# Kernel tuning notes

Hardware: AMD Instinct MI355X
Metric: run time of the kernel (lower is better)

The kernel has to match this reference:

```python
import jax, jax.numpy as jnp
import numpy as np


def lstm_step(x_t, h, c, Wih, Whh, bih, bhh):
    # PyTorch LSTM gate order: i, f, g, o
    gates = x_t @ Wih.T + h @ Whh.T + bih + bhh
    i, f, g, o = jnp.split(gates, 4, axis=-1)
    i = jax.nn.sigmoid(i)
    f = jax.nn.sigmoid(f)
    g = jnp.tanh(g)
    o = jax.nn.sigmoid(o)
    c_new = f * c + i * g
    h_new = o * jnp.tanh(c_new)
    return h_new, c_new


def setup_inputs() -> dict:
    key = jax.random.key(0)
    N, C, T, V, M = 512, 3, 300, 25, 2
    F = C * V * M  # 150
    H = 100
    ks = jax.random.split(key, 12)
    s = 1.0 / np.sqrt(H)  # PyTorch LSTM/Linear init scale
    u = lambda k, shape: jax.random.uniform(k, shape, jnp.float32, -s, s)
    return {
        "x": jax.random.normal(ks[0], (N, C, T, V, M), jnp.float32),
        "enc_Wih": u(ks[1], (4 * H, F)),
        "enc_Whh": u(ks[2], (4 * H, H)),
        "enc_bih": u(ks[3], (4 * H,)),
        "enc_bhh": u(ks[4], (4 * H,)),
        "dec_Wih": u(ks[5], (4 * H, F)),
        "dec_Whh": u(ks[6], (4 * H, H)),
        "dec_bih": u(ks[7], (4 * H,)),
        "dec_bhh": u(ks[8], (4 * H,)),
        "fc_W": u(ks[9], (F, H)),
        "fc_b": u(ks[10], (F,)),
    }


def reference(x, enc_Wih, enc_Whh, enc_bih, enc_bhh,
              dec_Wih, dec_Whh, dec_bih, dec_bhh, fc_W, fc_b):
    N, C, T, V, M = x.shape
    F = C * V * M
    H = enc_Whh.shape[1]
    # (N,C,T,V,M) -> (N,T,C*V*M)
    xs = jnp.transpose(x, (0, 2, 1, 3, 4)).reshape(N, T, F)

    # Encoder LSTM: only need final (h, c)
    h0 = jnp.zeros((N, H), x.dtype)
    c0 = jnp.zeros((N, H), x.dtype)

    def enc_step(carry, xt):
        h, c = carry
        h, c = lstm_step(xt, h, c, enc_Wih, enc_Whh, enc_bih, enc_bhh)
        return (h, c), None

    (h, c), _ = jax.lax.scan(enc_step, (h0, c0), jnp.swapaxes(xs, 0, 1))

    inp0 = jnp.zeros((N, F), x.dtype)

    def dec_step(carry, _):
        inp, h, c = carry
        h, c = lstm_step(inp, h, c, dec_Wih, dec_Whh, dec_bih, dec_bhh)
        out = h @ fc_W.T + fc_b
        return (out, h, c), out

    _, outs = jax.lax.scan(dec_step, (inp0, h, c), None, length=T - 1)  # [T-1,N,F]

    # outputs[:,0,:] stays zero, like the torch.zeros buffer
    outputs = jnp.concatenate([jnp.zeros((1, N, F), x.dtype), outs], axis=0)  # [T,N,F]
    outputs = jnp.swapaxes(outputs, 0, 1).reshape(N, T, C, V, M)
    return jnp.transpose(outputs, (0, 2, 1, 3, 4))  # (N,C,T,V,M)
```

## Files before the change

kernel.cpp:

```cpp
#include <hip/hip_runtime.h>
#include <hip/hip_fp16.h>


#define OFF_W2T   0
#define OFF_WDT   51200
#define OFF_WET   102400
#define OFF_PIH   153600
#define OFF_BENC  192000
#define OFF_B1    192512
#define OFF_BEFF  193024
#define OFF_HIST  193536
#define HIST_STRIDE 29952
#define OFF_XG    7861248

typedef _Float16 h2_t __attribute__((ext_vector_type(2)));

#if defined(__has_builtin)
#if __has_builtin(__builtin_amdgcn_fdot2)
#define HAS_FDOT2 1
#endif
#endif

__device__ __forceinline__ float fdot2u(unsigned a, unsigned b, float c) {
#ifdef HAS_FDOT2
  return __builtin_amdgcn_fdot2(__builtin_bit_cast(h2_t, a), __builtin_bit_cast(h2_t, b), c, false);
#else
  float al = __half2float(__ushort_as_half((unsigned short)(a & 0xffffu)));
  float ah = __half2float(__ushort_as_half((unsigned short)(a >> 16)));
  float bl = __half2float(__ushort_as_half((unsigned short)(b & 0xffffu)));
  float bh = __half2float(__ushort_as_half((unsigned short)(b >> 16)));
  return fmaf(ah, bh, fmaf(al, bl, c));
#endif
}

__device__ __forceinline__ float fast_sig(float x) {
  float e = __builtin_amdgcn_exp2f(x * -1.442695040888963f);
  return __builtin_amdgcn_rcpf(1.f + e);
}
__device__ __forceinline__ float fast_tanh(float x) {
  float e = __builtin_amdgcn_exp2f(x * -2.885390081777926f);
  return fmaf(2.f, __builtin_amdgcn_rcpf(1.f + e), -1.f);
}

__device__ __forceinline__ float lstm_tail(float acc, int ty, float& c) {
  float v1 = __shfl_xor(acc, 1);
  float v2 = __shfl_xor(acc, 2);
  float v3 = __shfl_xor(v1, 2);
  float d0 = acc;
  float iv = (ty==0)?d0:(ty==1)?v1:(ty==2)?v2:v3;
  float fv = (ty==1)?d0:(ty==0)?v1:(ty==3)?v2:v3;
  float gv = (ty==2)?d0:(ty==3)?v1:(ty==0)?v2:v3;
  float ov = (ty==3)?d0:(ty==2)?v1:(ty==1)?v2:v3;
  float fi = fast_sig(iv), ff = fast_sig(fv), fo = fast_sig(ov);
  float fg = fast_tanh(gv);
  c = fmaf(ff, c, fi * fg);
  return fo * fast_tanh(c);
}

__global__ void prep(const float* __restrict__ dWih, const float* __restrict__ dWhh,
                     const float* __restrict__ dbih, const float* __restrict__ dbhh,
                     const float* __restrict__ eWih, const float* __restrict__ eWhh,
                     const float* __restrict__ ebih, const float* __restrict__ ebhh,
                     const float* __restrict__ fcW,  const float* __restrict__ fcb,
                     float* __restrict__ ws)
{
  int idx = blockIdx.x * 256 + threadIdx.x;
  if (idx < 51200) {
    int j = idx >> 9, t = idx & 511;
    float w2 = 0.f, wd = 0.f, we = 0.f;
    if (t < 400) {
      int r = (t & 3) * 100 + (t >> 2);
      float s = dWhh[r * 100 + j];
      float acc = 0.f;
      for (int f = 0; f < 150; ++f) acc = fmaf(dWih[r * 150 + f], fcW[f * 100 + j], acc);
      w2 = s + acc; wd = s; we = eWhh[r * 100 + j];
    }
    ws[OFF_W2T + idx] = w2; ws[OFF_WDT + idx] = wd; ws[OFF_WET + idx] = we;
  } else if (idx < 51200 + 38400) {
    int k = idx - 51200; int d = k >> 9, t = k & 511;
    unsigned pk = 0;
    if (t < 400) {
      int r = (t & 3) * 100 + (t >> 2);
      unsigned lo = __half_as_ushort(__float2half(eWih[r * 150 + 2 * d]));
      unsigned hi = __half_as_ushort(__float2half(eWih[r * 150 + 2 * d + 1]));
      pk = lo | (hi << 16);
    }
    ((unsigned*)ws)[OFF_PIH + k] = pk;
  } else if (idx < 51200 + 38400 + 512) {
    int t = idx - (51200 + 38400);
    float be = 0.f, b1 = 0.f, bf = 0.f;
    if (t < 400) {
      int r = (t & 3) * 100 + (t >> 2);
      be = ebih[r] + ebhh[r];
      b1 = dbih[r] + dbhh[r];
      float acc = 0.f;
      for (int f = 0; f < 150; ++f) acc = fmaf(dWih[r * 150 + f], fcb[f], acc);
      bf = b1 + acc;
    }
    ws[OFF_BENC + t] = be; ws[OFF_B1 + t] = b1; ws[OFF_BEFF + t] = bf;
  }
}

__global__ __launch_bounds__(512, 4)
void pre(const float* __restrict__ x, const float* __restrict__ ws,
         unsigned short* __restrict__ xg, int n0)
{
  const int tid = threadIdx.x;
  const int n = n0 + blockIdx.x;
  __shared__ unsigned short xls[150 * 160];

  unsigned wih[75];
  const unsigned* pih = ((const unsigned*)ws) + OFF_PIH;
#pragma unroll
  for (int d = 0; d < 75; ++d) wih[d] = pih[(d << 9) + tid];

  const float* xb = x + (size_t)n * 45000;
  unsigned short* xgr = xg + (size_t)blockIdx.x * 120000 + ((tid < 400) ? tid : 0);
  const bool on = tid < 400;

  for (int phase = 0; phase < 2; ++phase) {
    const int tbase = phase * 150;
    if (phase) __syncthreads();
    for (int d = tid; d < 150 * 160; d += 512) {
      int tl = d / 160, f = d - tl * 160;
      float v = 0.f;
      if (f < 150) {
        int c = f / 50, q = f - c * 50;
        v = xb[c * 15000 + (tbase + tl) * 50 + q];
      }
      xls[tl * 160 + f] = __half_as_ushort(__float2half(v));
    }
    __syncthreads();
    if (on) {
      for (int tl = 0; tl < 150; ++tl) {
        const uint4* row = (const uint4*)(xls + tl * 160);
        float a = 0.f;
#pragma unroll
        for (int ch = 0; ch < 18; ++ch) {
          uint4 v = row[ch];
          a = fdot2u(wih[4 * ch + 0], v.x, a);
          a = fdot2u(wih[4 * ch + 1], v.y, a);
          a = fdot2u(wih[4 * ch + 2], v.z, a);
          a = fdot2u(wih[4 * ch + 3], v.w, a);
        }
        uint4 v = row[18];
        a = fdot2u(wih[72], v.x, a);
        a = fdot2u(wih[73], v.y, a);
        a = fdot2u(wih[74], v.z, a);
        xgr[(size_t)(tbase + tl) * 400] = __half_as_ushort(__float2half(a));
      }
    }
  }
}

__global__ __launch_bounds__(512, 4)
void recurrent(const unsigned short* __restrict__ xg, float* __restrict__ ws, int n0)
{
  const int t  = threadIdx.x;
  const int n  = n0 + blockIdx.x;
  const int j  = t >> 2, ty = t & 3;
  const bool leader = (t < 400) && (ty == 0);
  __shared__ float hbuf[2][112];

  float whh[100];
#pragma unroll
  for (int k = 0; k < 100; ++k) whh[k] = ws[OFF_WET + (k << 9) + t];

  const float benc  = ws[OFF_BENC + t];
  const float b1g   = ws[OFF_B1   + t];
  const float beffg = ws[OFF_BEFF + t];
  unsigned short* histn = ((unsigned short*)(ws + OFF_HIST)) + (size_t)n * HIST_STRIDE;
  const unsigned short* xgr = xg + (size_t)blockIdx.x * 120000 + ((t < 400) ? t : 0);
  float c = 0.f;

  unsigned short p0 = xgr[0], p1 = xgr[400];
  for (int ts = 0; ts < 300; ++ts) {
    const int rd = ts & 1, wr = rd ^ 1;
    const int pi = (ts + 2 < 300) ? (ts + 2) : 299;
    unsigned short nx = xgr[(size_t)pi * 400];
    float acc = benc + __half2float(__ushort_as_half(p0));
    if (ts > 0) {
#pragma unroll
      for (int k = 0; k < 100; k += 4) {
        float4 h4 = *(const float4*)&hbuf[rd][k];
        acc = fmaf(whh[k+0], h4.x, acc);
        acc = fmaf(whh[k+1], h4.y, acc);
        acc = fmaf(whh[k+2], h4.z, acc);
        acc = fmaf(whh[k+3], h4.w, acc);
      }
    }
    float hn = lstm_tail(acc, ty, c);
    if (leader) hbuf[wr][j] = hn;
    __syncthreads();
    p0 = p1; p1 = nx;
  }

#pragma unroll
  for (int k = 0; k < 100; ++k) whh[k] = ws[OFF_WDT + (k << 9) + t];
  for (int s = 1; s <= 299; ++s) {
    const int rd = (299 + s) & 1, wr = rd ^ 1;
    float acc = (s == 1) ? b1g : beffg;
#pragma unroll
    for (int k = 0; k < 100; k += 4) {
      float4 h4 = *(const float4*)&hbuf[rd][k];
      acc = fmaf(whh[k+0], h4.x, acc);
      acc = fmaf(whh[k+1], h4.y, acc);
      acc = fmaf(whh[k+2], h4.z, acc);
      acc = fmaf(whh[k+3], h4.w, acc);
    }
    float hn = lstm_tail(acc, ty, c);
    if (leader) {
      hbuf[wr][j] = hn;
      histn[(s - 1) * 100 + j] = __half_as_ushort(__float2half(hn));
    }
    __syncthreads();
    if (s == 1) {
#pragma unroll
      for (int k = 0; k < 100; ++k) whh[k] = ws[OFF_W2T + (k << 9) + t];
    }
  }
}

__global__ __launch_bounds__(192, 4)
void emit(const float* __restrict__ ws, const float* __restrict__ fcW,
          const float* __restrict__ fcb, float* __restrict__ out)
{
  const int f = threadIdx.x;
  const int n = blockIdx.x;
  const int z = blockIdx.y;
  __shared__ unsigned short hl[15008];

  const uint4* src = (const uint4*)(((const unsigned short*)(ws + OFF_HIST)) +
                                    (size_t)n * HIST_STRIDE + z * 15000);
  for (int k = f; k < 1875; k += 192) ((uint4*)hl)[k] = src[k];

  const bool on = f < 150;
  unsigned fw[50];
  float bias = 0.f;
  if (on) {
    const float* fp = fcW + f * 100;
#pragma unroll
    for (int q = 0; q < 50; ++q) {
      unsigned lo = __half_as_ushort(__float2half(fp[2*q]));
      unsigned hi = __half_as_ushort(__float2half(fp[2*q+1]));
      fw[q] = lo | (hi << 16);
    }
    bias = fcb[f];
  }
  __syncthreads();

  if (!on) return;
  const int cc = f / 50, r = f - cc * 50;
  float* ob = out + (size_t)n * 45000 + cc * 15000 + r;
  if (z == 0) ob[0] = 0.f;
  const int rows = z ? 149 : 150;
  for (int tl = 0; tl < rows; ++tl) {
    const uint4* row = (const uint4*)(hl + tl * 100);
    float acc = bias;
#pragma unroll
    for (int ch = 0; ch < 12; ++ch) {
      uint4 v = row[ch];
      acc = fdot2u(fw[4*ch+0], v.x, acc);
      acc = fdot2u(fw[4*ch+1], v.y, acc);
      acc = fdot2u(fw[4*ch+2], v.z, acc);
      acc = fdot2u(fw[4*ch+3], v.w, acc);
    }
    uint2 v2 = *(const uint2*)(hl + tl * 100 + 96);
    acc = fdot2u(fw[48], v2.x, acc);
    acc = fdot2u(fw[49], v2.y, acc);
    const int tt = z * 150 + tl + 1;
    ob[tt * 50] = acc;
  }
}

extern "C" void kernel_launch(void* const* d_in, const int* in_sizes, int n_in,
                              void* d_out, int out_size, void* d_ws, size_t ws_size,
                              hipStream_t stream) {
  const float* x    = (const float*)d_in[0];
  const float* eWih = (const float*)d_in[1];
  const float* eWhh = (const float*)d_in[2];
  const float* ebih = (const float*)d_in[3];
  const float* ebhh = (const float*)d_in[4];
  const float* dWih = (const float*)d_in[5];
  const float* dWhh = (const float*)d_in[6];
  const float* dbih = (const float*)d_in[7];
  const float* dbhh = (const float*)d_in[8];
  const float* fcW  = (const float*)d_in[9];
  const float* fcb  = (const float*)d_in[10];
  float* out = (float*)d_out;
  float* ws  = (float*)d_ws;

  const size_t fixed_bytes = (size_t)OFF_XG * 4;
  int npass = 1;
  while (npass < 8) {
    size_t need = fixed_bytes + (size_t)(512 / npass) * 300 * 400 * 2;
    if (need <= ws_size) break;
    npass *= 2;
  }
  const int chunk = 512 / npass;
  unsigned short* xg = (unsigned short*)((char*)d_ws + fixed_bytes);

  prep<<<352, 256, 0, stream>>>(dWih, dWhh, dbih, dbhh, eWih, eWhh, ebih, ebhh, fcW, fcb, ws);
  for (int p = 0; p < npass; ++p) {
    pre<<<chunk, 512, 0, stream>>>(x, ws, xg, p * chunk);
    recurrent<<<chunk, 512, 0, stream>>>(xg, ws, p * chunk);
  }
  emit<<<dim3(512, 2), 192, 0, stream>>>(ws, fcW, fcb, out);
}
```

Baseline: 1.325 ms.

## Use packed fp16 dot2 for recurrent matvec and split accumulators

Recurrent weights are stored as packed fp16 pairs and the hidden state is kept in fp16 shared memory, so each step's 100-wide matvec uses fdot2 with four independent accumulators instead of 100 serial fp32 FMAs. The LSTM tail now applies the gate nonlinearity once per lane before shuffling, instead of every lane computing all four. The first encoder step and first decoder step are peeled out of their loops, and the pre and emit dot products also get split accumulators. This halves weight register use and shortens the serial dependency chain on the per-step critical path. The cost is fp16 rounding of the hidden state and weights across 600 recurrent steps, which can build up error.

```diff
diff --git a/kernel.cpp b/kernel.cpp
--- a/kernel.cpp
+++ b/kernel.cpp
@@ -2,16 +2,16 @@
 #include <hip/hip_fp16.h>
 
 
-#define OFF_W2T   0
-#define OFF_WDT   51200
-#define OFF_WET   102400
-#define OFF_PIH   153600
-#define OFF_BENC  192000
-#define OFF_B1    192512
-#define OFF_BEFF  193024
-#define OFF_HIST  193536
+#define B_W2P   0u
+#define B_WDP   102400u
+#define B_WEP   204800u
+#define B_PIH   307200u
+#define B_BENC  460800u
+#define B_B1    462848u
+#define B_BEFF  464896u
+#define B_HIST  466944u
 #define HIST_STRIDE 29952
-#define OFF_XG    7861248
+#define B_XG    31137792u
 
 typedef _Float16 h2_t __attribute__((ext_vector_type(2)));
 
@@ -33,6 +33,11 @@
 #endif
 }
 
+__device__ __forceinline__ unsigned pack2f(float a, float b) {
+  return (unsigned)__half_as_ushort(__float2half(a)) |
+         ((unsigned)__half_as_ushort(__float2half(b)) << 16);
+}
+
 __device__ __forceinline__ float fast_sig(float x) {
   float e = __builtin_amdgcn_exp2f(x * -1.442695040888963f);
   return __builtin_amdgcn_rcpf(1.f + e);
@@ -43,18 +48,31 @@
 }
 
 __device__ __forceinline__ float lstm_tail(float acc, int ty, float& c) {
-  float v1 = __shfl_xor(acc, 1);
-  float v2 = __shfl_xor(acc, 2);
+  float sg = fast_sig(acc);
+  float th = fast_tanh(acc);
+  float act = (ty == 2) ? th : sg;
+  float v1 = __shfl_xor(act, 1);
+  float v2 = __shfl_xor(act, 2);
   float v3 = __shfl_xor(v1, 2);
-  float d0 = acc;
-  float iv = (ty==0)?d0:(ty==1)?v1:(ty==2)?v2:v3;
-  float fv = (ty==1)?d0:(ty==0)?v1:(ty==3)?v2:v3;
-  float gv = (ty==2)?d0:(ty==3)?v1:(ty==0)?v2:v3;
-  float ov = (ty==3)?d0:(ty==2)?v1:(ty==1)?v2:v3;
-  float fi = fast_sig(iv), ff = fast_sig(fv), fo = fast_sig(ov);
-  float fg = fast_tanh(gv);
-  c = fmaf(ff, c, fi * fg);
-  return fo * fast_tanh(c);
+  c = fmaf(v1, c, act * v2);
+  return v3 * fast_tanh(c);
+}
+
+__device__ __forceinline__ float dot100(const unsigned short* hb, const unsigned* wp) {
+  const uint4* h4 = (const uint4*)hb;
+  float a0 = 0.f, a1 = 0.f, a2 = 0.f, a3 = 0.f;
+#pragma unroll
+  for (int ch = 0; ch < 12; ++ch) {
+    uint4 v = h4[ch];
+    a0 = fdot2u(wp[4 * ch + 0], v.x, a0);
+    a1 = fdot2u(wp[4 * ch + 1], v.y, a1);
+    a2 = fdot2u(wp[4 * ch + 2], v.z, a2);
+    a3 = fdot2u(wp[4 * ch + 3], v.w, a3);
+  }
+  uint2 v2 = *(const uint2*)(hb + 96);
+  a0 = fdot2u(wp[48], v2.x, a0);
+  a1 = fdot2u(wp[49], v2.y, a1);
+  return (a0 + a1) + (a2 + a3);
 }
 
 __global__ void prep(const float* __restrict__ dWih, const float* __restrict__ dWhh,
@@ -62,32 +80,40 @@
                      const float* __restrict__ eWih, const float* __restrict__ eWhh,
                      const float* __restrict__ ebih, const float* __restrict__ ebhh,
                      const float* __restrict__ fcW,  const float* __restrict__ fcb,
-                     float* __restrict__ ws)
+                     char* __restrict__ wsb)
 {
   int idx = blockIdx.x * 256 + threadIdx.x;
-  if (idx < 51200) {
-    int j = idx >> 9, t = idx & 511;
-    float w2 = 0.f, wd = 0.f, we = 0.f;
+  if (idx < 25600) {
+    int q = idx >> 9, t = idx & 511;
+    unsigned w2p = 0, wdp = 0, wep = 0;
     if (t < 400) {
       int r = (t & 3) * 100 + (t >> 2);
-      float s = dWhh[r * 100 + j];
-      float acc = 0.f;
-      for (int f = 0; f < 150; ++f) acc = fmaf(dWih[r * 150 + f], fcW[f * 100 + j], acc);
-      w2 = s + acc; wd = s; we = eWhh[r * 100 + j];
-    }
-    ws[OFF_W2T + idx] = w2; ws[OFF_WDT + idx] = wd; ws[OFF_WET + idx] = we;
-  } else if (idx < 51200 + 38400) {
-    int k = idx - 51200; int d = k >> 9, t = k & 511;
+      int j0 = 2 * q, j1 = 2 * q + 1;
+      float wd0 = dWhh[r * 100 + j0], wd1 = dWhh[r * 100 + j1];
+      float we0 = eWhh[r * 100 + j0], we1 = eWhh[r * 100 + j1];
+      float s0 = 0.f, s1 = 0.f;
+      for (int f = 0; f < 150; ++f) {
+        float a = dWih[r * 150 + f];
+        s0 = fmaf(a, fcW[f * 100 + j0], s0);
+        s1 = fmaf(a, fcW[f * 100 + j1], s1);
+      }
+      w2p = pack2f(wd0 + s0, wd1 + s1);
+      wdp = pack2f(wd0, wd1);
+      wep = pack2f(we0, we1);
+    }
+    ((unsigned*)(wsb + B_W2P))[idx] = w2p;
+    ((unsigned*)(wsb + B_WDP))[idx] = wdp;
+    ((unsigned*)(wsb + B_WEP))[idx] = wep;
+  } else if (idx < 25600 + 38400) {
+    int k = idx - 25600; int d = k >> 9, t = k & 511;
     unsigned pk = 0;
     if (t < 400) {
       int r = (t & 3) * 100 + (t >> 2);
-      unsigned lo = __half_as_ushort(__float2half(eWih[r * 150 + 2 * d]));
-      unsigned hi = __half_as_ushort(__float2half(eWih[r * 150 + 2 * d + 1]));
-      pk = lo | (hi << 16);
-    }
-    ((unsigned*)ws)[OFF_PIH + k] = pk;
-  } else if (idx < 51200 + 38400 + 512) {
-    int t = idx - (51200 + 38400);
+      pk = pack2f(eWih[r * 150 + 2 * d], eWih[r * 150 + 2 * d + 1]);
+    }
+    ((unsigned*)(wsb + B_PIH))[k] = pk;
+  } else if (idx < 25600 + 38400 + 512) {
+    int t = idx - (25600 + 38400);
     float be = 0.f, b1 = 0.f, bf = 0.f;
     if (t < 400) {
       int r = (t & 3) * 100 + (t >> 2);
@@ -97,12 +123,14 @@
       for (int f = 0; f < 150; ++f) acc = fmaf(dWih[r * 150 + f], fcb[f], acc);
       bf = b1 + acc;
     }
-    ws[OFF_BENC + t] = be; ws[OFF_B1 + t] = b1; ws[OFF_BEFF + t] = bf;
+    ((float*)(wsb + B_BENC))[t] = be;
+    ((float*)(wsb + B_B1))[t]   = b1;
+    ((float*)(wsb + B_BEFF))[t] = bf;
   }
 }
 
 __global__ __launch_bounds__(512, 4)
-void pre(const float* __restrict__ x, const float* __restrict__ ws,
+void pre(const float* __restrict__ x, const char* __restrict__ wsb,
          unsigned short* __restrict__ xg, int n0)
 {
   const int tid = threadIdx.x;
@@ -110,7 +138,7 @@
   __shared__ unsigned short xls[150 * 160];
 
   unsigned wih[75];
-  const unsigned* pih = ((const unsigned*)ws) + OFF_PIH;
+  const unsigned* pih = (const unsigned*)(wsb + B_PIH);
 #pragma unroll
   for (int d = 0; d < 75; ++d) wih[d] = pih[(d << 9) + tid];
 
@@ -134,19 +162,20 @@
     if (on) {
       for (int tl = 0; tl < 150; ++tl) {
         const uint4* row = (const uint4*)(xls + tl * 160);
-        float a = 0.f;
+        float a0 = 0.f, a1 = 0.f, a2 = 0.f, a3 = 0.f;
 #pragma unroll
         for (int ch = 0; ch < 18; ++ch) {
           uint4 v = row[ch];
-          a = fdot2u(wih[4 * ch + 0], v.x, a);
-          a = fdot2u(wih[4 * ch + 1], v.y, a);
-          a = fdot2u(wih[4 * ch + 2], v.z, a);
-          a = fdot2u(wih[4 * ch + 3], v.w, a);
+          a0 = fdot2u(wih[4 * ch + 0], v.x, a0);
+          a1 = fdot2u(wih[4 * ch + 1], v.y, a1);
+          a2 = fdot2u(wih[4 * ch + 2], v.z, a2);
+          a3 = fdot2u(wih[4 * ch + 3], v.w, a3);
         }
         uint4 v = row[18];
-        a = fdot2u(wih[72], v.x, a);
-        a = fdot2u(wih[73], v.y, a);
-        a = fdot2u(wih[74], v.z, a);
+        a0 = fdot2u(wih[72], v.x, a0);
+        a1 = fdot2u(wih[73], v.y, a1);
+        a2 = fdot2u(wih[74], v.z, a2);
+        float a = (a0 + a1) + (a2 + a3);
         xgr[(size_t)(tbase + tl) * 400] = __half_as_ushort(__float2half(a));
       }
     }
@@ -154,75 +183,73 @@
 }
 
 __global__ __launch_bounds__(512, 4)
-void recurrent(const unsigned short* __restrict__ xg, float* __restrict__ ws, int n0)
+void recurrent(const unsigned short* __restrict__ xg, char* __restrict__ wsb, int n0)
 {
   const int t  = threadIdx.x;
   const int n  = n0 + blockIdx.x;
   const int j  = t >> 2, ty = t & 3;
   const bool leader = (t < 400) && (ty == 0);
-  __shared__ float hbuf[2][112];
-
-  float whh[100];
-#pragma unroll
-  for (int k = 0; k < 100; ++k) whh[k] = ws[OFF_WET + (k << 9) + t];
-
-  const float benc  = ws[OFF_BENC + t];
-  const float b1g   = ws[OFF_B1   + t];
-  const float beffg = ws[OFF_BEFF + t];
-  unsigned short* histn = ((unsigned short*)(ws + OFF_HIST)) + (size_t)n * HIST_STRIDE;
+  __shared__ unsigned short hh[2][112];
+
+  const unsigned* WEP = (const unsigned*)(wsb + B_WEP);
+  const unsigned* WDP = (const unsigned*)(wsb + B_WDP);
+  const unsigned* W2P = (const unsigned*)(wsb + B_W2P);
+
+  unsigned wp[50];
+#pragma unroll
+  for (int q = 0; q < 50; ++q) wp[q] = WEP[(q << 9) + t];
+
+  const float benc = ((const float*)(wsb + B_BENC))[t];
+  const float b1g  = ((const float*)(wsb + B_B1))[t];
+  const float beff = ((const float*)(wsb + B_BEFF))[t];
+  unsigned short* histn = (unsigned short*)(wsb + B_HIST) + (size_t)n * HIST_STRIDE;
   const unsigned short* xgr = xg + (size_t)blockIdx.x * 120000 + ((t < 400) ? t : 0);
   float c = 0.f;
 
-  unsigned short p0 = xgr[0], p1 = xgr[400];
-  for (int ts = 0; ts < 300; ++ts) {
+  unsigned short p1 = xgr[400];
+  {
+    float acc = benc + __half2float(__ushort_as_half(xgr[0]));
+    float hn = lstm_tail(acc, ty, c);
+    if (leader) hh[1][j] = __half_as_ushort(__float2half(hn));
+    __syncthreads();
+  }
+  for (int ts = 1; ts < 300; ++ts) {
     const int rd = ts & 1, wr = rd ^ 1;
-    const int pi = (ts + 2 < 300) ? (ts + 2) : 299;
-    unsigned short nx = xgr[(size_t)pi * 400];
-    float acc = benc + __half2float(__ushort_as_half(p0));
-    if (ts > 0) {
-#pragma unroll
-      for (int k = 0; k < 100; k += 4) {
-        float4 h4 = *(const float4*)&hbuf[rd][k];
-        acc = fmaf(whh[k+0], h4.x, acc);
-        acc = fmaf(whh[k+1], h4.y, acc);
-        acc = fmaf(whh[k+2], h4.z, acc);
-        acc = fmaf(whh[k+3], h4.w, acc);
-      }
-    }
+    unsigned short pn = xgr[(size_t)((ts + 1 < 300) ? ts + 1 : 299) * 400];
+    float acc = benc + __half2float(__ushort_as_half(p1)) + dot100(hh[rd], wp);
     float hn = lstm_tail(acc, ty, c);
-    if (leader) hbuf[wr][j] = hn;
-    __syncthreads();
-    p0 = p1; p1 = nx;
-  }
-
-#pragma unroll
-  for (int k = 0; k < 100; ++k) whh[k] = ws[OFF_WDT + (k << 9) + t];
-  for (int s = 1; s <= 299; ++s) {
-    const int rd = (299 + s) & 1, wr = rd ^ 1;
-    float acc = (s == 1) ? b1g : beffg;
-#pragma unroll
-    for (int k = 0; k < 100; k += 4) {
-      float4 h4 = *(const float4*)&hbuf[rd][k];
-      acc = fmaf(whh[k+0], h4.x, acc);
-      acc = fmaf(whh[k+1], h4.y, acc);
-      acc = fmaf(whh[k+2], h4.z, acc);
-      acc = fmaf(whh[k+3], h4.w, acc);
-    }
+    if (leader) hh[wr][j] = __half_as_ushort(__float2half(hn));
+    __syncthreads();
+    p1 = pn;
+  }
+
+#pragma unroll
+  for (int q = 0; q < 50; ++q) wp[q] = WDP[(q << 9) + t];
+  {
+    float acc = b1g + dot100(hh[0], wp);
     float hn = lstm_tail(acc, ty, c);
     if (leader) {
-      hbuf[wr][j] = hn;
+      hh[1][j] = __half_as_ushort(__float2half(hn));
+      histn[j] = __half_as_ushort(__float2half(hn));
+    }
+    __syncthreads();
+  }
+#pragma unroll
+  for (int q = 0; q < 50; ++q) wp[q] = W2P[(q << 9) + t];
+  for (int s = 2; s <= 299; ++s) {
+    const int rd = (299 + s) & 1, wr = rd ^ 1;
+    float acc = beff + dot100(hh[rd], wp);
+    float hn = lstm_tail(acc, ty, c);
+    if (leader) {
+      hh[wr][j] = __half_as_ushort(__float2half(hn));
       histn[(s - 1) * 100 + j] = __half_as_ushort(__float2half(hn));
     }
     __syncthreads();
-    if (s == 1) {
-#pragma unroll
-      for (int k = 0; k < 100; ++k) whh[k] = ws[OFF_W2T + (k << 9) + t];
-    }
   }
 }
 
 __global__ __launch_bounds__(192, 4)
-void emit(const float* __restrict__ ws, const float* __restrict__ fcW,
+void emit(const char* __restrict__ wsb, const float* __restrict__ fcW,
           const float* __restrict__ fcb, float* __restrict__ out)
 {
   const int f = threadIdx.x;
@@ -230,7 +257,7 @@
   const int z = blockIdx.y;
   __shared__ unsigned short hl[15008];
 
-  const uint4* src = (const uint4*)(((const unsigned short*)(ws + OFF_HIST)) +
+  const uint4* src = (const uint4*)((const unsigned short*)(wsb + B_HIST) +
                                     (size_t)n * HIST_STRIDE + z * 15000);
   for (int k = f; k < 1875; k += 192) ((uint4*)hl)[k] = src[k];
 
@@ -240,11 +267,7 @@
   if (on) {
     const float* fp = fcW + f * 100;
 #pragma unroll
-    for (int q = 0; q < 50; ++q) {
-      unsigned lo = __half_as_ushort(__float2half(fp[2*q]));
-      unsigned hi = __half_as_ushort(__float2half(fp[2*q+1]));
-      fw[q] = lo | (hi << 16);
-    }
+    for (int q = 0; q < 50; ++q) fw[q] = pack2f(fp[2 * q], fp[2 * q + 1]);
     bias = fcb[f];
   }
   __syncthreads();
@@ -256,20 +279,20 @@
   const int rows = z ? 149 : 150;
   for (int tl = 0; tl < rows; ++tl) {
     const uint4* row = (const uint4*)(hl + tl * 100);
-    float acc = bias;
+    float a0 = bias, a1 = 0.f, a2 = 0.f, a3 = 0.f;
 #pragma unroll
     for (int ch = 0; ch < 12; ++ch) {
       uint4 v = row[ch];
-      acc = fdot2u(fw[4*ch+0], v.x, acc);
-      acc = fdot2u(fw[4*ch+1], v.y, acc);
-      acc = fdot2u(fw[4*ch+2], v.z, acc);
-      acc = fdot2u(fw[4*ch+3], v.w, acc);
+      a0 = fdot2u(fw[4 * ch + 0], v.x, a0);
+      a1 = fdot2u(fw[4 * ch + 1], v.y, a1);
+      a2 = fdot2u(fw[4 * ch + 2], v.z, a2);
+      a3 = fdot2u(fw[4 * ch + 3], v.w, a3);
     }
     uint2 v2 = *(const uint2*)(hl + tl * 100 + 96);
-    acc = fdot2u(fw[48], v2.x, acc);
-    acc = fdot2u(fw[49], v2.y, acc);
+    a0 = fdot2u(fw[48], v2.x, a0);
+    a1 = fdot2u(fw[49], v2.y, a1);
     const int tt = z * 150 + tl + 1;
-    ob[tt * 50] = acc;
+    ob[tt * 50] = (a0 + a1) + (a2 + a3);
   }
 }
 
@@ -288,22 +311,21 @@
   const float* fcW  = (const float*)d_in[9];
   const float* fcb  = (const float*)d_in[10];
   float* out = (float*)d_out;
-  float* ws  = (float*)d_ws;
-
-  const size_t fixed_bytes = (size_t)OFF_XG * 4;
+  char* wsb  = (char*)d_ws;
+
   int npass = 1;
   while (npass < 8) {
-    size_t need = fixed_bytes + (size_t)(512 / npass) * 300 * 400 * 2;
+    size_t need = (size_t)B_XG + (size_t)(512 / npass) * 300 * 400 * 2;
     if (need <= ws_size) break;
     npass *= 2;
   }
   const int chunk = 512 / npass;
-  unsigned short* xg = (unsigned short*)((char*)d_ws + fixed_bytes);
-
-  prep<<<352, 256, 0, stream>>>(dWih, dWhh, dbih, dbhh, eWih, eWhh, ebih, ebhh, fcW, fcb, ws);
+  unsigned short* xg = (unsigned short*)(wsb + B_XG);
+
+  prep<<<252, 256, 0, stream>>>(dWih, dWhh, dbih, dbhh, eWih, eWhh, ebih, ebhh, fcW, fcb, wsb);
   for (int p = 0; p < npass; ++p) {
-    pre<<<chunk, 512, 0, stream>>>(x, ws, xg, p * chunk);
-    recurrent<<<chunk, 512, 0, stream>>>(xg, ws, p * chunk);
-  }
-  emit<<<dim3(512, 2), 192, 0, stream>>>(ws, fcW, fcb, out);
-}
+    pre<<<chunk, 512, 0, stream>>>(x, wsb, xg, p * chunk);
+    recurrent<<<chunk, 512, 0, stream>>>(xg, wsb, p * chunk);
+  }
+  emit<<<dim3(512, 2), 192, 0, stream>>>(wsb, fcW, fcb, out);
+}
```

Result: faster. 1.136 ms (-14.3%).
